# Kernel tuning notes

Measured on AMD Instinct MI355X. Metric: run time of the kernel, lower is better.

The kernel has to match this reference:

```python
import jax, jax.numpy as jnp
import numpy as np

B, S, D_IN, D_OUT = 4, 2048, 2048, 2048
E, R = 8, 8
SCALING = 16.0 / 8.0  # lora_alpha / r
# Dropout (p=0.05) treated as identity (eval mode) for a deterministic reference.

def setup_inputs() -> dict:
    key = jax.random.key(0)
    ks = jax.random.split(key, 8)
    x = jax.random.normal(ks[0], (B, S, D_IN), dtype=jnp.float32)
    base_W = jax.random.normal(ks[1], (D_OUT, D_IN), dtype=jnp.float32) * 0.02
    base_b = jax.random.normal(ks[2], (D_OUT,), dtype=jnp.float32) * 0.02
    shared_A = jax.random.normal(ks[3], (R, D_IN), dtype=jnp.float32) * 0.01
    shared_B = jax.random.normal(ks[4], (D_OUT, R), dtype=jnp.float32) * 0.01
    expert_A = jax.random.normal(ks[5], (E, R, D_IN), dtype=jnp.float32) * 0.01
    expert_B = jax.random.normal(ks[6], (E, D_OUT, R), dtype=jnp.float32) * 0.01
    task_emb = jax.random.normal(ks[7], (E, D_IN), dtype=jnp.float32) * 0.01
    collab_w = jnp.array(0.5, dtype=jnp.float32)
    return {"x": x, "base_W": base_W, "base_b": base_b,
            "shared_A": shared_A, "shared_B": shared_B,
            "expert_A": expert_A, "expert_B": expert_B,
            "task_emb": task_emb, "collab_w": collab_w}

def reference(x, base_W, base_b, shared_A, shared_B, expert_A, expert_B, task_emb, collab_w):
    # base linear: [B,S,D_out]
    base_out = jnp.einsum('bsi,oi->bso', x, base_W) + base_b
    # shared LoRA path
    shared_out = jnp.einsum('bsr,or->bso', jnp.einsum('bsi,ri->bsr', x, shared_A), shared_B) * SCALING
    # soft routing over task experts (task_id=None branch)
    x_mean = x.mean(axis=1)                               # [B,D_in]
    routing = jax.nn.softmax(x_mean @ task_emb.T, axis=-1)  # [B,E]
    t = jnp.einsum('bsi,eri->bser', x, expert_A)          # [B,S,E,R] low-rank
    task_out = jnp.einsum('bser,eor,be->bso', t, expert_B, routing) * SCALING
    cw = jax.nn.sigmoid(collab_w)
    return base_out + cw * shared_out + (1.0 - cw) * task_out
```

## Files before the change

kernel.cpp:

```cpp
#include <hip/hip_runtime.h>
#include <hip/hip_bf16.h>
#include <math.h>

#define BATCH 4
#define SEQ   2048
#define DIN   2048
#define DOUT  2048
#define NEXP  8
#define RANK  8
#define MTOT  (BATCH * SEQ)
#define KE    64

typedef __bf16 bf16x8 __attribute__((ext_vector_type(8)));
typedef __bf16 bf16x4 __attribute__((ext_vector_type(4)));
typedef float  f32x4  __attribute__((ext_vector_type(4)));

#define GLOBAL_AS __attribute__((address_space(1)))
#define LDS_AS    __attribute__((address_space(3)))

__global__ __launch_bounds__(256) void prep_all(
    const float* __restrict__ x, const float* __restrict__ W,
    const float* __restrict__ expert_A, const float* __restrict__ shared_A,
    const float* __restrict__ expert_B, const float* __restrict__ shared_B,
    const float* __restrict__ collab,
    __bf16* __restrict__ xb, float* __restrict__ partial,
    __bf16* __restrict__ Wb, __bf16* __restrict__ caug, __bf16* __restrict__ Ab)
{
    const int bid = blockIdx.x;
    const int t = threadIdx.x;
    if (bid < 1024) {
        const int dc = bid & 3, sc = (bid >> 2) & 63, b = bid >> 8;
        const int i = dc * 512 + t * 2;
        size_t base = ((size_t)b * SEQ + (size_t)sc * 32) * DIN + i;
        float a0 = 0.f, a1 = 0.f;
        for (int s = 0; s < 32; ++s) {
            float2 v = *(const float2*)&x[base + (size_t)s * DIN];
            a0 += v.x; a1 += v.y;
            __bf16 h0 = (__bf16)v.x, h1 = (__bf16)v.y;
            ((__bf16*)&xb[base + (size_t)s * DIN])[0] = h0;
            ((__bf16*)&xb[base + (size_t)s * DIN])[1] = h1;
        }
        float2 p = { a0, a1 };
        *(float2*)&partial[((size_t)b * 64 + sc) * DIN + i] = p;
    } else if (bid < 5120) {
        int idx = (bid - 1024) * 1024 + t * 4;
        int o = idx >> 11, i = idx & 2047;
        float cw = 1.0f / (1.0f + expf(-collab[0]));
        float s = cw * 2.0f;
        float4 w = *(const float4*)&W[idx];
        float dx = 0.f, dy = 0.f, dz = 0.f, dw = 0.f;
        #pragma unroll
        for (int r = 0; r < 8; ++r) {
            float bs = shared_B[(size_t)o * RANK + r];
            float4 as = *(const float4*)&shared_A[(size_t)r * DIN + i];
            dx += bs * as.x; dy += bs * as.y; dz += bs * as.z; dw += bs * as.w;
        }
        bf16x4 h = { (__bf16)(w.x + s * dx), (__bf16)(w.y + s * dy),
                     (__bf16)(w.z + s * dz), (__bf16)(w.w + s * dw) };
        *(bf16x4*)&Wb[idx] = h;
    } else if (bid < 5632) {
        int idx = (bid - 5120) * 256 + t;
        int k = idx & 63, o = idx >> 6;
        float cw = 1.0f / (1.0f + expf(-collab[0]));
        caug[idx] = (__bf16)((1.0f - cw) * 2.0f *
            expert_B[((size_t)(k >> 3) * DOUT + o) * RANK + (k & 7)]);
    } else {
        int idx = (bid - 5632) * 1024 + t * 4;
        float4 v = *(const float4*)&expert_A[idx];
        bf16x4 h = { (__bf16)v.x, (__bf16)v.y, (__bf16)v.z, (__bf16)v.w };
        *(bf16x4*)&Ab[idx] = h;
    }
}

__global__ __launch_bounds__(256) void gemm_t_rout(
    const __bf16* __restrict__ xb, const __bf16* __restrict__ Ab,
    const float* __restrict__ partial, const float* __restrict__ task_emb,
    __bf16* __restrict__ pt, float* __restrict__ routing)
{
    __shared__ __bf16 lsA[128 * 32];
    __shared__ __bf16 lsB[64 * 32];
    __shared__ float red[256];
    const int bid = blockIdx.x;
    const int t = threadIdx.x;

    if (bid >= 256) {
        const int b = bid - 256;
        float xm[8] = {0.f,0.f,0.f,0.f,0.f,0.f,0.f,0.f};
        for (int sc = 0; sc < 64; ++sc) {
            const float* pp = partial + ((size_t)b * 64 + sc) * DIN + t * 8;
            float4 v0 = *(const float4*)pp, v1 = *(const float4*)(pp + 4);
            xm[0] += v0.x; xm[1] += v0.y; xm[2] += v0.z; xm[3] += v0.w;
            xm[4] += v1.x; xm[5] += v1.y; xm[6] += v1.z; xm[7] += v1.w;
        }
        float le[NEXP];
        #pragma unroll
        for (int e = 0; e < NEXP; ++e) {
            const float* te = task_emb + (size_t)e * DIN + t * 8;
            float4 u0 = *(const float4*)te, u1 = *(const float4*)(te + 4);
            le[e] = xm[0]*u0.x + xm[1]*u0.y + xm[2]*u0.z + xm[3]*u0.w
                  + xm[4]*u1.x + xm[5]*u1.y + xm[6]*u1.z + xm[7]*u1.w;
        }
        __shared__ float logits[NEXP];
        for (int e = 0; e < NEXP; ++e) {
            red[t] = le[e];
            __syncthreads();
            for (int s = 128; s > 0; s >>= 1) {
                if (t < s) red[t] += red[t + s];
                __syncthreads();
            }
            if (t == 0) logits[e] = red[0] * (1.0f / (float)SEQ);
            __syncthreads();
        }
        if (t == 0) {
            float mx = logits[0];
            for (int e = 1; e < NEXP; ++e) mx = fmaxf(mx, logits[e]);
            float ex[NEXP], den = 0.f;
            for (int e = 0; e < NEXP; ++e) { ex[e] = expf(logits[e] - mx); den += ex[e]; }
            for (int e = 0; e < NEXP; ++e) routing[b * NEXP + e] = ex[e] / den;
        }
        return;
    }

    const int lane = t & 63;
    const int w = t >> 6;
    const int kc = bid & 3;
    const int m0 = (bid >> 2) * 128;

    f32x4 acc[2][4];
    #pragma unroll
    for (int a = 0; a < 2; ++a)
        #pragma unroll
        for (int c = 0; c < 4; ++c) acc[a][c] = (f32x4){0.f, 0.f, 0.f, 0.f};

    for (int k0 = kc * 512; k0 < kc * 512 + 512; k0 += 32) {
        #pragma unroll
        for (int q = 0; q < 2; ++q) {
            int L = q * 256 + t;
            int row = L >> 2, seg = L & 3;
            const __bf16* gpA = xb + (size_t)(m0 + row) * DIN + k0 + seg * 8;
            int Lu = q * 256 + (t & ~63);
            __builtin_amdgcn_global_load_lds((GLOBAL_AS void*)gpA,
                (LDS_AS void*)&lsA[Lu * 8], 16, 0, 0);
        }
        {
            int row = t >> 2, seg = t & 3;
            const __bf16* gpB = Ab + (size_t)row * DIN + k0 + seg * 8;
            __builtin_amdgcn_global_load_lds((GLOBAL_AS void*)gpB,
                (LDS_AS void*)&lsB[(t & ~63) * 8], 16, 0, 0);
        }
        __syncthreads();
        bf16x8 af[2], bfr[4];
        #pragma unroll
        for (int tm = 0; tm < 2; ++tm)
            af[tm] = *(const bf16x8*)&lsA[(w * 32 + tm * 16 + (lane & 15)) * 32 + (lane >> 4) * 8];
        #pragma unroll
        for (int tn = 0; tn < 4; ++tn)
            bfr[tn] = *(const bf16x8*)&lsB[(tn * 16 + (lane & 15)) * 32 + (lane >> 4) * 8];
        #pragma unroll
        for (int tm = 0; tm < 2; ++tm)
            #pragma unroll
            for (int tn = 0; tn < 4; ++tn)
                acc[tm][tn] = __builtin_amdgcn_mfma_f32_16x16x32_bf16(
                    af[tm], bfr[tn], acc[tm][tn], 0, 0, 0);
        __syncthreads();
    }
    #pragma unroll
    for (int tm = 0; tm < 2; ++tm)
        #pragma unroll
        for (int tn = 0; tn < 4; ++tn) {
            int col = tn * 16 + (lane & 15);
            #pragma unroll
            for (int v = 0; v < 4; ++v) {
                int row = m0 + w * 32 + tm * 16 + (lane >> 4) * 4 + v;
                pt[((size_t)kc * MTOT + row) * KE + col] = (__bf16)acc[tm][tn][v];
            }
        }
}

__global__ __launch_bounds__(256) void reduce_route(
    const __bf16* __restrict__ pt, const float* __restrict__ routing,
    __bf16* __restrict__ tb)
{
    size_t idx = ((size_t)blockIdx.x * 256 + threadIdx.x) * 4;
    int k0 = (int)(idx & 63);
    int m  = (int)(idx >> 6);
    int b  = m >> 11;
    float f = routing[b * NEXP + (k0 >> 3)];
    float sx = 0.f, sy = 0.f, sz = 0.f, sw = 0.f;
    #pragma unroll
    for (int kc = 0; kc < 4; ++kc) {
        bf16x4 v = *(const bf16x4*)&pt[(size_t)kc * MTOT * KE + idx];
        sx += (float)v[0]; sy += (float)v[1]; sz += (float)v[2]; sw += (float)v[3];
    }
    bf16x4 h = { (__bf16)(sx * f), (__bf16)(sy * f), (__bf16)(sz * f), (__bf16)(sw * f) };
    *(bf16x4*)&tb[idx] = h;
}

__global__ __launch_bounds__(256) void gemm_main(
    const __bf16* __restrict__ xb, const __bf16* __restrict__ Wb,
    const __bf16* __restrict__ tb, const __bf16* __restrict__ caug,
    const float* __restrict__ bias, float* __restrict__ out)
{
    __shared__ __bf16 lsA[128 * 64];
    __shared__ __bf16 lsB[128 * 64];
    const int t = threadIdx.x;
    const int lane = t & 63;
    const int wm = (t >> 6) >> 1, wn = (t >> 6) & 1;
    const int m0 = blockIdx.x * 128;
    const int n0 = blockIdx.y * 128;

    int rowq[4], segq[4], ldso[4];
    #pragma unroll
    for (int q = 0; q < 4; ++q) {
        rowq[q] = q * 32 + (t >> 3);
        segq[q] = (t & 7) ^ (rowq[q] & 7);
        ldso[q] = (q * 256 + (t & ~63)) * 8;
    }
    const __bf16* pA[4]; const __bf16* pB[4];
    #pragma unroll
    for (int q = 0; q < 4; ++q) {
        pA[q] = xb + (size_t)(m0 + rowq[q]) * DIN + segq[q] * 8;
        pB[q] = Wb + (size_t)(n0 + rowq[q]) * DIN + segq[q] * 8;
    }
    int aoff[2][4], boff[2][4];
    #pragma unroll
    for (int tm = 0; tm < 4; ++tm) {
        int r = wm * 64 + tm * 16 + (lane & 15);
        #pragma unroll
        for (int kk = 0; kk < 2; ++kk)
            aoff[kk][tm] = r * 64 + (((kk * 4 + (lane >> 4)) ^ (r & 7)) * 8);
    }
    #pragma unroll
    for (int tn = 0; tn < 4; ++tn) {
        int r = wn * 64 + tn * 16 + (lane & 15);
        #pragma unroll
        for (int kk = 0; kk < 2; ++kk)
            boff[kk][tn] = r * 64 + (((kk * 4 + (lane >> 4)) ^ (r & 7)) * 8);
    }

    f32x4 acc[4][4];
    #pragma unroll
    for (int a = 0; a < 4; ++a)
        #pragma unroll
        for (int c = 0; c < 4; ++c) acc[a][c] = (f32x4){0.f, 0.f, 0.f, 0.f};

    for (int it = 0; it < 32; ++it) {
        #pragma unroll
        for (int q = 0; q < 4; ++q) {
            __builtin_amdgcn_global_load_lds((GLOBAL_AS void*)pA[q],
                (LDS_AS void*)&lsA[ldso[q]], 16, 0, 0);
            __builtin_amdgcn_global_load_lds((GLOBAL_AS void*)pB[q],
                (LDS_AS void*)&lsB[ldso[q]], 16, 0, 0);
            pA[q] += 64; pB[q] += 64;
        }
        __syncthreads();
        #pragma unroll
        for (int kk = 0; kk < 2; ++kk) {
            bf16x8 af[4], bfr[4];
            #pragma unroll
            for (int tm = 0; tm < 4; ++tm) af[tm]  = *(const bf16x8*)&lsA[aoff[kk][tm]];
            #pragma unroll
            for (int tn = 0; tn < 4; ++tn) bfr[tn] = *(const bf16x8*)&lsB[boff[kk][tn]];
            #pragma unroll
            for (int tm = 0; tm < 4; ++tm)
                #pragma unroll
                for (int tn = 0; tn < 4; ++tn)
                    acc[tm][tn] = __builtin_amdgcn_mfma_f32_16x16x32_bf16(
                        af[tm], bfr[tn], acc[tm][tn], 0, 0, 0);
        }
        __syncthreads();
    }

    {
        #pragma unroll
        for (int q = 0; q < 4; ++q) {
            const __bf16* qA = tb   + (size_t)(m0 + rowq[q]) * KE + segq[q] * 8;
            const __bf16* qB = caug + (size_t)(n0 + rowq[q]) * KE + segq[q] * 8;
            __builtin_amdgcn_global_load_lds((GLOBAL_AS void*)qA,
                (LDS_AS void*)&lsA[ldso[q]], 16, 0, 0);
            __builtin_amdgcn_global_load_lds((GLOBAL_AS void*)qB,
                (LDS_AS void*)&lsB[ldso[q]], 16, 0, 0);
        }
        __syncthreads();
        #pragma unroll
        for (int kk = 0; kk < 2; ++kk) {
            bf16x8 af[4], bfr[4];
            #pragma unroll
            for (int tm = 0; tm < 4; ++tm) af[tm]  = *(const bf16x8*)&lsA[aoff[kk][tm]];
            #pragma unroll
            for (int tn = 0; tn < 4; ++tn) bfr[tn] = *(const bf16x8*)&lsB[boff[kk][tn]];
            #pragma unroll
            for (int tm = 0; tm < 4; ++tm)
                #pragma unroll
                for (int tn = 0; tn < 4; ++tn)
                    acc[tm][tn] = __builtin_amdgcn_mfma_f32_16x16x32_bf16(
                        af[tm], bfr[tn], acc[tm][tn], 0, 0, 0);
        }
        __syncthreads();
    }

    #pragma unroll
    for (int tm = 0; tm < 4; ++tm)
        #pragma unroll
        for (int tn = 0; tn < 4; ++tn) {
            int col = n0 + wn * 64 + tn * 16 + (lane & 15);
            float bv = bias[col];
            #pragma unroll
            for (int v = 0; v < 4; ++v) {
                int row = m0 + wm * 64 + tm * 16 + (lane >> 4) * 4 + v;
                out[(size_t)row * DOUT + col] = acc[tm][tn][v] + bv;
            }
        }
}

extern "C" void kernel_launch(void* const* d_in, const int* in_sizes, int n_in,
                              void* d_out, int out_size, void* d_ws, size_t ws_size,
                              hipStream_t stream)
{
    const float* x        = (const float*)d_in[0];
    const float* base_W   = (const float*)d_in[1];
    const float* base_b   = (const float*)d_in[2];
    const float* shared_A = (const float*)d_in[3];
    const float* shared_B = (const float*)d_in[4];
    const float* expert_A = (const float*)d_in[5];
    const float* expert_B = (const float*)d_in[6];
    const float* task_emb = (const float*)d_in[7];
    const float* collab_w = (const float*)d_in[8];
    float* out = (float*)d_out;

    char* ws = (char*)d_ws;
    __bf16* xb      = (__bf16*)(ws + 0);
    __bf16* Wb      = (__bf16*)(ws + 33554432);
    __bf16* pt      = (__bf16*)(ws + 41943040);
    __bf16* tb      = (__bf16*)(ws + 46137344);
    __bf16* caug    = (__bf16*)(ws + 47185920);
    __bf16* Ab      = (__bf16*)(ws + 47448064);
    float*  partial = (float*) (ws + 47710208);
    float*  routing = (float*) (ws + 49807360);

    prep_all    <<<dim3(5760), 256, 0, stream>>>(x, base_W, expert_A, shared_A,
                                                 expert_B, shared_B, collab_w,
                                                 xb, partial, Wb, caug, Ab);
    gemm_t_rout <<<dim3(260), 256, 0, stream>>>(xb, Ab, partial, task_emb, pt, routing);
    reduce_route<<<dim3(512), 256, 0, stream>>>(pt, routing, tb);
    gemm_main   <<<dim3(64, 16), 256, 0, stream>>>(xb, Wb, tb, caug, base_b, out);
}
```

Before: 242.4 us.

## Fold routing logits into low-rank GEMM and fuse reduce into main GEMM

Drops the separate x-mean pass and routing block. task_emb is appended as extra rows of the low-rank A matrix, so routing logits fall out of the t-GEMM by linearity and are accumulated with atomics. The reduce_route kernel is removed: gemm_main sums the four split-K partials, computes the softmax and scales the A fragments in registers before the expert MFMA step. The low-rank GEMM also moves to a 64-wide K tile with swizzled LDS, and the x conversion is vectorised. One launch and several intermediate buffers go away, at the cost of an extra memset, atomics, and bf16 precision for the mean/logit path.

```diff
diff --git a/kernel.cpp b/kernel.cpp
--- a/kernel.cpp
+++ b/kernel.cpp
@@ -10,6 +10,7 @@
 #define RANK  8
 #define MTOT  (BATCH * SEQ)
 #define KE    64
+#define KAB   96
 
 typedef __bf16 bf16x8 __attribute__((ext_vector_type(8)));
 typedef __bf16 bf16x4 __attribute__((ext_vector_type(4)));
@@ -22,29 +23,25 @@
     const float* __restrict__ x, const float* __restrict__ W,
     const float* __restrict__ expert_A, const float* __restrict__ shared_A,
     const float* __restrict__ expert_B, const float* __restrict__ shared_B,
-    const float* __restrict__ collab,
-    __bf16* __restrict__ xb, float* __restrict__ partial,
-    __bf16* __restrict__ Wb, __bf16* __restrict__ caug, __bf16* __restrict__ Ab)
+    const float* __restrict__ task_emb, const float* __restrict__ collab,
+    __bf16* __restrict__ xb, __bf16* __restrict__ Wb,
+    __bf16* __restrict__ caug, __bf16* __restrict__ Ab)
 {
     const int bid = blockIdx.x;
     const int t = threadIdx.x;
-    if (bid < 1024) {
-        const int dc = bid & 3, sc = (bid >> 2) & 63, b = bid >> 8;
-        const int i = dc * 512 + t * 2;
-        size_t base = ((size_t)b * SEQ + (size_t)sc * 32) * DIN + i;
-        float a0 = 0.f, a1 = 0.f;
-        for (int s = 0; s < 32; ++s) {
-            float2 v = *(const float2*)&x[base + (size_t)s * DIN];
-            a0 += v.x; a1 += v.y;
-            __bf16 h0 = (__bf16)v.x, h1 = (__bf16)v.y;
-            ((__bf16*)&xb[base + (size_t)s * DIN])[0] = h0;
-            ((__bf16*)&xb[base + (size_t)s * DIN])[1] = h1;
-        }
-        float2 p = { a0, a1 };
-        *(float2*)&partial[((size_t)b * 64 + sc) * DIN + i] = p;
-    } else if (bid < 5120) {
-        int idx = (bid - 1024) * 1024 + t * 4;
-        int o = idx >> 11, i = idx & 2047;
+    if (bid < 2048) {
+        size_t base = (size_t)bid * 8192 + (size_t)t * 32;
+        #pragma unroll
+        for (int j = 0; j < 4; ++j) {
+            float4 v0 = *(const float4*)&x[base + j * 8];
+            float4 v1 = *(const float4*)&x[base + j * 8 + 4];
+            bf16x8 h = { (__bf16)v0.x, (__bf16)v0.y, (__bf16)v0.z, (__bf16)v0.w,
+                         (__bf16)v1.x, (__bf16)v1.y, (__bf16)v1.z, (__bf16)v1.w };
+            *(bf16x8*)&xb[base + j * 8] = h;
+        }
+    } else if (bid < 6144) {
+        size_t idx = (size_t)(bid - 2048) * 1024 + t * 4;
+        int o = (int)(idx >> 11), i = (int)(idx & 2047);
         float cw = 1.0f / (1.0f + expf(-collab[0]));
         float s = cw * 2.0f;
         float4 w = *(const float4*)&W[idx];
@@ -58,112 +55,99 @@
         bf16x4 h = { (__bf16)(w.x + s * dx), (__bf16)(w.y + s * dy),
                      (__bf16)(w.z + s * dz), (__bf16)(w.w + s * dw) };
         *(bf16x4*)&Wb[idx] = h;
-    } else if (bid < 5632) {
-        int idx = (bid - 5120) * 256 + t;
-        int k = idx & 63, o = idx >> 6;
+    } else if (bid < 6272) {
+        int idx = (bid - 6144) * 1024 + t * 4;
+        int o = idx >> 6, k = idx & 63;
         float cw = 1.0f / (1.0f + expf(-collab[0]));
-        caug[idx] = (__bf16)((1.0f - cw) * 2.0f *
-            expert_B[((size_t)(k >> 3) * DOUT + o) * RANK + (k & 7)]);
+        float s = (1.0f - cw) * 2.0f;
+        float4 v = *(const float4*)&expert_B[((size_t)(k >> 3) * DOUT + o) * RANK + (k & 7)];
+        bf16x4 h = { (__bf16)(s * v.x), (__bf16)(s * v.y),
+                     (__bf16)(s * v.z), (__bf16)(s * v.w) };
+        *(bf16x4*)&caug[idx] = h;
     } else {
-        int idx = (bid - 5632) * 1024 + t * 4;
-        float4 v = *(const float4*)&expert_A[idx];
-        bf16x4 h = { (__bf16)v.x, (__bf16)v.y, (__bf16)v.z, (__bf16)v.w };
-        *(bf16x4*)&Ab[idx] = h;
+        int row = bid - 6272;
+        int c = t * 8;
+        bf16x8 h = { (__bf16)0.f, (__bf16)0.f, (__bf16)0.f, (__bf16)0.f,
+                     (__bf16)0.f, (__bf16)0.f, (__bf16)0.f, (__bf16)0.f };
+        if (row < 64) {
+            float4 v0 = *(const float4*)&expert_A[(size_t)row * DIN + c];
+            float4 v1 = *(const float4*)&expert_A[(size_t)row * DIN + c + 4];
+            h = bf16x8{ (__bf16)v0.x, (__bf16)v0.y, (__bf16)v0.z, (__bf16)v0.w,
+                        (__bf16)v1.x, (__bf16)v1.y, (__bf16)v1.z, (__bf16)v1.w };
+        } else if (row < 72) {
+            float4 v0 = *(const float4*)&task_emb[(size_t)(row - 64) * DIN + c];
+            float4 v1 = *(const float4*)&task_emb[(size_t)(row - 64) * DIN + c + 4];
+            h = bf16x8{ (__bf16)v0.x, (__bf16)v0.y, (__bf16)v0.z, (__bf16)v0.w,
+                        (__bf16)v1.x, (__bf16)v1.y, (__bf16)v1.z, (__bf16)v1.w };
+        }
+        *(bf16x8*)&Ab[(size_t)row * DIN + c] = h;
     }
 }
 
-__global__ __launch_bounds__(256) void gemm_t_rout(
+__global__ __launch_bounds__(256) void gemm_t(
     const __bf16* __restrict__ xb, const __bf16* __restrict__ Ab,
-    const float* __restrict__ partial, const float* __restrict__ task_emb,
-    __bf16* __restrict__ pt, float* __restrict__ routing)
+    __bf16* __restrict__ pt, float* __restrict__ logits)
 {
-    __shared__ __bf16 lsA[128 * 32];
-    __shared__ __bf16 lsB[64 * 32];
-    __shared__ float red[256];
+    __shared__ __bf16 lsA[128 * 64];
+    __shared__ __bf16 lsB[KAB * 64];
+    __shared__ float lsc[32];
     const int bid = blockIdx.x;
     const int t = threadIdx.x;
-
-    if (bid >= 256) {
-        const int b = bid - 256;
-        float xm[8] = {0.f,0.f,0.f,0.f,0.f,0.f,0.f,0.f};
-        for (int sc = 0; sc < 64; ++sc) {
-            const float* pp = partial + ((size_t)b * 64 + sc) * DIN + t * 8;
-            float4 v0 = *(const float4*)pp, v1 = *(const float4*)(pp + 4);
-            xm[0] += v0.x; xm[1] += v0.y; xm[2] += v0.z; xm[3] += v0.w;
-            xm[4] += v1.x; xm[5] += v1.y; xm[6] += v1.z; xm[7] += v1.w;
-        }
-        float le[NEXP];
-        #pragma unroll
-        for (int e = 0; e < NEXP; ++e) {
-            const float* te = task_emb + (size_t)e * DIN + t * 8;
-            float4 u0 = *(const float4*)te, u1 = *(const float4*)(te + 4);
-            le[e] = xm[0]*u0.x + xm[1]*u0.y + xm[2]*u0.z + xm[3]*u0.w
-                  + xm[4]*u1.x + xm[5]*u1.y + xm[6]*u1.z + xm[7]*u1.w;
-        }
-        __shared__ float logits[NEXP];
-        for (int e = 0; e < NEXP; ++e) {
-            red[t] = le[e];
-            __syncthreads();
-            for (int s = 128; s > 0; s >>= 1) {
-                if (t < s) red[t] += red[t + s];
-                __syncthreads();
-            }
-            if (t == 0) logits[e] = red[0] * (1.0f / (float)SEQ);
-            __syncthreads();
-        }
-        if (t == 0) {
-            float mx = logits[0];
-            for (int e = 1; e < NEXP; ++e) mx = fmaxf(mx, logits[e]);
-            float ex[NEXP], den = 0.f;
-            for (int e = 0; e < NEXP; ++e) { ex[e] = expf(logits[e] - mx); den += ex[e]; }
-            for (int e = 0; e < NEXP; ++e) routing[b * NEXP + e] = ex[e] / den;
-        }
-        return;
-    }
-
     const int lane = t & 63;
     const int w = t >> 6;
     const int kc = bid & 3;
     const int m0 = (bid >> 2) * 128;
-
-    f32x4 acc[2][4];
+    const int b  = bid >> 6;
+
+    f32x4 acc[2][5];
     #pragma unroll
     for (int a = 0; a < 2; ++a)
         #pragma unroll
-        for (int c = 0; c < 4; ++c) acc[a][c] = (f32x4){0.f, 0.f, 0.f, 0.f};
-
-    for (int k0 = kc * 512; k0 < kc * 512 + 512; k0 += 32) {
-        #pragma unroll
-        for (int q = 0; q < 2; ++q) {
-            int L = q * 256 + t;
-            int row = L >> 2, seg = L & 3;
-            const __bf16* gpA = xb + (size_t)(m0 + row) * DIN + k0 + seg * 8;
-            int Lu = q * 256 + (t & ~63);
-            __builtin_amdgcn_global_load_lds((GLOBAL_AS void*)gpA,
-                (LDS_AS void*)&lsA[Lu * 8], 16, 0, 0);
-        }
-        {
-            int row = t >> 2, seg = t & 3;
-            const __bf16* gpB = Ab + (size_t)row * DIN + k0 + seg * 8;
-            __builtin_amdgcn_global_load_lds((GLOBAL_AS void*)gpB,
-                (LDS_AS void*)&lsB[(t & ~63) * 8], 16, 0, 0);
-        }
-        __syncthreads();
-        bf16x8 af[2], bfr[4];
-        #pragma unroll
-        for (int tm = 0; tm < 2; ++tm)
-            af[tm] = *(const bf16x8*)&lsA[(w * 32 + tm * 16 + (lane & 15)) * 32 + (lane >> 4) * 8];
-        #pragma unroll
-        for (int tn = 0; tn < 4; ++tn)
-            bfr[tn] = *(const bf16x8*)&lsB[(tn * 16 + (lane & 15)) * 32 + (lane >> 4) * 8];
-        #pragma unroll
-        for (int tm = 0; tm < 2; ++tm)
-            #pragma unroll
-            for (int tn = 0; tn < 4; ++tn)
-                acc[tm][tn] = __builtin_amdgcn_mfma_f32_16x16x32_bf16(
-                    af[tm], bfr[tn], acc[tm][tn], 0, 0, 0);
-        __syncthreads();
-    }
+        for (int c = 0; c < 5; ++c) acc[a][c] = (f32x4){0.f, 0.f, 0.f, 0.f};
+
+    for (int k0 = kc * 512; k0 < kc * 512 + 512; k0 += 64) {
+        #pragma unroll
+        for (int q = 0; q < 4; ++q) {
+            int G = q * 256 + t;
+            int row = G >> 3, sl = G & 7, seg = sl ^ (row & 7);
+            const __bf16* gp = xb + (size_t)(m0 + row) * DIN + k0 + seg * 8;
+            __builtin_amdgcn_global_load_lds((GLOBAL_AS void*)gp,
+                (LDS_AS void*)&lsA[(q * 256 + (t & ~63)) * 8], 16, 0, 0);
+        }
+        #pragma unroll
+        for (int q = 0; q < 3; ++q) {
+            int G = q * 256 + t;
+            int row = G >> 3, sl = G & 7, seg = sl ^ (row & 7);
+            const __bf16* gp = Ab + (size_t)row * DIN + k0 + seg * 8;
+            __builtin_amdgcn_global_load_lds((GLOBAL_AS void*)gp,
+                (LDS_AS void*)&lsB[(q * 256 + (t & ~63)) * 8], 16, 0, 0);
+        }
+        __syncthreads();
+        #pragma unroll
+        for (int kk = 0; kk < 2; ++kk) {
+            bf16x8 af[2], bfr[5];
+            #pragma unroll
+            for (int tm = 0; tm < 2; ++tm) {
+                int r = w * 32 + tm * 16 + (lane & 15);
+                int slot = (kk * 4 + (lane >> 4)) ^ (r & 7);
+                af[tm] = *(const bf16x8*)&lsA[r * 64 + slot * 8];
+            }
+            #pragma unroll
+            for (int tn = 0; tn < 5; ++tn) {
+                int r = tn * 16 + (lane & 15);
+                int slot = (kk * 4 + (lane >> 4)) ^ (r & 7);
+                bfr[tn] = *(const bf16x8*)&lsB[r * 64 + slot * 8];
+            }
+            #pragma unroll
+            for (int tm = 0; tm < 2; ++tm)
+                #pragma unroll
+                for (int tn = 0; tn < 5; ++tn)
+                    acc[tm][tn] = __builtin_amdgcn_mfma_f32_16x16x32_bf16(
+                        af[tm], bfr[tn], acc[tm][tn], 0, 0, 0);
+        }
+        __syncthreads();
+    }
+
     #pragma unroll
     for (int tm = 0; tm < 2; ++tm)
         #pragma unroll
@@ -175,31 +159,27 @@
                 pt[((size_t)kc * MTOT + row) * KE + col] = (__bf16)acc[tm][tn][v];
             }
         }
-}
-
-__global__ __launch_bounds__(256) void reduce_route(
-    const __bf16* __restrict__ pt, const float* __restrict__ routing,
-    __bf16* __restrict__ tb)
-{
-    size_t idx = ((size_t)blockIdx.x * 256 + threadIdx.x) * 4;
-    int k0 = (int)(idx & 63);
-    int m  = (int)(idx >> 6);
-    int b  = m >> 11;
-    float f = routing[b * NEXP + (k0 >> 3)];
-    float sx = 0.f, sy = 0.f, sz = 0.f, sw = 0.f;
-    #pragma unroll
-    for (int kc = 0; kc < 4; ++kc) {
-        bf16x4 v = *(const bf16x4*)&pt[(size_t)kc * MTOT * KE + idx];
-        sx += (float)v[0]; sy += (float)v[1]; sz += (float)v[2]; sw += (float)v[3];
-    }
-    bf16x4 h = { (__bf16)(sx * f), (__bf16)(sy * f), (__bf16)(sz * f), (__bf16)(sw * f) };
-    *(bf16x4*)&tb[idx] = h;
+
+    float s = 0.f;
+    #pragma unroll
+    for (int tm = 0; tm < 2; ++tm)
+        #pragma unroll
+        for (int v = 0; v < 4; ++v) s += acc[tm][4][v];
+    s += __shfl_down(s, 32);
+    s += __shfl_down(s, 16);
+    if (lane < 8) lsc[w * 8 + lane] = s;
+    __syncthreads();
+    if (t < 8) {
+        float tot = lsc[t] + lsc[8 + t] + lsc[16 + t] + lsc[24 + t];
+        atomicAdd(&logits[b * NEXP + t], tot);
+    }
 }
 
 __global__ __launch_bounds__(256) void gemm_main(
     const __bf16* __restrict__ xb, const __bf16* __restrict__ Wb,
-    const __bf16* __restrict__ tb, const __bf16* __restrict__ caug,
-    const float* __restrict__ bias, float* __restrict__ out)
+    const __bf16* __restrict__ pt, const __bf16* __restrict__ caug,
+    const float* __restrict__ logits, const float* __restrict__ bias,
+    float* __restrict__ out)
 {
     __shared__ __bf16 lsA[128 * 64];
     __shared__ __bf16 lsB[128 * 64];
@@ -208,6 +188,23 @@
     const int wm = (t >> 6) >> 1, wn = (t >> 6) & 1;
     const int m0 = blockIdx.x * 128;
     const int n0 = blockIdx.y * 128;
+    const int b  = m0 >> 11;
+
+    float f[NEXP];
+    {
+        float li[NEXP];
+        #pragma unroll
+        for (int e = 0; e < NEXP; ++e) li[e] = logits[b * NEXP + e] * (1.0f / (float)SEQ);
+        float mx = li[0];
+        #pragma unroll
+        for (int e = 1; e < NEXP; ++e) mx = fmaxf(mx, li[e]);
+        float den = 0.f;
+        #pragma unroll
+        for (int e = 0; e < NEXP; ++e) { f[e] = expf(li[e] - mx); den += f[e]; }
+        float rden = 1.0f / den;
+        #pragma unroll
+        for (int e = 0; e < NEXP; ++e) f[e] *= rden;
+    }
 
     int rowq[4], segq[4], ldso[4];
     #pragma unroll
@@ -216,34 +213,74 @@
         segq[q] = (t & 7) ^ (rowq[q] & 7);
         ldso[q] = (q * 256 + (t & ~63)) * 8;
     }
+    int aoff[2][4], boff[2][4];
+    #pragma unroll
+    for (int tm = 0; tm < 4; ++tm) {
+        int r = wm * 64 + tm * 16 + (lane & 15);
+        #pragma unroll
+        for (int kk = 0; kk < 2; ++kk)
+            aoff[kk][tm] = r * 64 + (((kk * 4 + (lane >> 4)) ^ (r & 7)) * 8);
+    }
+    #pragma unroll
+    for (int tn = 0; tn < 4; ++tn) {
+        int r = wn * 64 + tn * 16 + (lane & 15);
+        #pragma unroll
+        for (int kk = 0; kk < 2; ++kk)
+            boff[kk][tn] = r * 64 + (((kk * 4 + (lane >> 4)) ^ (r & 7)) * 8);
+    }
+
+    f32x4 acc[4][4];
+    #pragma unroll
+    for (int a = 0; a < 4; ++a)
+        #pragma unroll
+        for (int c = 0; c < 4; ++c) acc[a][c] = (f32x4){0.f, 0.f, 0.f, 0.f};
+
+    {
+        #pragma unroll
+        for (int q = 0; q < 4; ++q) {
+            const __bf16* gp = caug + (size_t)(n0 + rowq[q]) * KE + segq[q] * 8;
+            __builtin_amdgcn_global_load_lds((GLOBAL_AS void*)gp,
+                (LDS_AS void*)&lsB[ldso[q]], 16, 0, 0);
+        }
+        __syncthreads();
+        #pragma unroll
+        for (int kk = 0; kk < 2; ++kk) {
+            float fe = f[kk * 4 + (lane >> 4)];
+            bf16x8 afc[4], bfr[4];
+            #pragma unroll
+            for (int tm = 0; tm < 4; ++tm) {
+                int rm = m0 + wm * 64 + tm * 16 + (lane & 15);
+                int kb = kk * 32 + (lane >> 4) * 8;
+                const __bf16* p0 = pt + (size_t)rm * KE + kb;
+                bf16x8 v0 = *(const bf16x8*)(p0);
+                bf16x8 v1 = *(const bf16x8*)(p0 + (size_t)MTOT * KE);
+                bf16x8 v2 = *(const bf16x8*)(p0 + (size_t)2 * MTOT * KE);
+                bf16x8 v3 = *(const bf16x8*)(p0 + (size_t)3 * MTOT * KE);
+                bf16x8 r;
+                #pragma unroll
+                for (int j = 0; j < 8; ++j)
+                    r[j] = (__bf16)(((float)v0[j] + (float)v1[j] +
+                                     (float)v2[j] + (float)v3[j]) * fe);
+                afc[tm] = r;
+            }
+            #pragma unroll
+            for (int tn = 0; tn < 4; ++tn) bfr[tn] = *(const bf16x8*)&lsB[boff[kk][tn]];
+            #pragma unroll
+            for (int tm = 0; tm < 4; ++tm)
+                #pragma unroll
+                for (int tn = 0; tn < 4; ++tn)
+                    acc[tm][tn] = __builtin_amdgcn_mfma_f32_16x16x32_bf16(
+                        afc[tm], bfr[tn], acc[tm][tn], 0, 0, 0);
+        }
+        __syncthreads();
+    }
+
     const __bf16* pA[4]; const __bf16* pB[4];
     #pragma unroll
     for (int q = 0; q < 4; ++q) {
         pA[q] = xb + (size_t)(m0 + rowq[q]) * DIN + segq[q] * 8;
         pB[q] = Wb + (size_t)(n0 + rowq[q]) * DIN + segq[q] * 8;
     }
-    int aoff[2][4], boff[2][4];
-    #pragma unroll
-    for (int tm = 0; tm < 4; ++tm) {
-        int r = wm * 64 + tm * 16 + (lane & 15);
-        #pragma unroll
-        for (int kk = 0; kk < 2; ++kk)
-            aoff[kk][tm] = r * 64 + (((kk * 4 + (lane >> 4)) ^ (r & 7)) * 8);
-    }
-    #pragma unroll
-    for (int tn = 0; tn < 4; ++tn) {
-        int r = wn * 64 + tn * 16 + (lane & 15);
-        #pragma unroll
-        for (int kk = 0; kk < 2; ++kk)
-            boff[kk][tn] = r * 64 + (((kk * 4 + (lane >> 4)) ^ (r & 7)) * 8);
-    }
-
-    f32x4 acc[4][4];
-    #pragma unroll
-    for (int a = 0; a < 4; ++a)
-        #pragma unroll
-        for (int c = 0; c < 4; ++c) acc[a][c] = (f32x4){0.f, 0.f, 0.f, 0.f};
-
     for (int it = 0; it < 32; ++it) {
         #pragma unroll
         for (int q = 0; q < 4; ++q) {
@@ -252,34 +289,6 @@
             __builtin_amdgcn_global_load_lds((GLOBAL_AS void*)pB[q],
                 (LDS_AS void*)&lsB[ldso[q]], 16, 0, 0);
             pA[q] += 64; pB[q] += 64;
-        }
-        __syncthreads();
-        #pragma unroll
-        for (int kk = 0; kk < 2; ++kk) {
-            bf16x8 af[4], bfr[4];
-            #pragma unroll
-            for (int tm = 0; tm < 4; ++tm) af[tm]  = *(const bf16x8*)&lsA[aoff[kk][tm]];
-            #pragma unroll
-            for (int tn = 0; tn < 4; ++tn) bfr[tn] = *(const bf16x8*)&lsB[boff[kk][tn]];
-            #pragma unroll
-            for (int tm = 0; tm < 4; ++tm)
-                #pragma unroll
-                for (int tn = 0; tn < 4; ++tn)
-                    acc[tm][tn] = __builtin_amdgcn_mfma_f32_16x16x32_bf16(
-                        af[tm], bfr[tn], acc[tm][tn], 0, 0, 0);
-        }
-        __syncthreads();
-    }
-
-    {
-        #pragma unroll
-        for (int q = 0; q < 4; ++q) {
-            const __bf16* qA = tb   + (size_t)(m0 + rowq[q]) * KE + segq[q] * 8;
-            const __bf16* qB = caug + (size_t)(n0 + rowq[q]) * KE + segq[q] * 8;
-            __builtin_amdgcn_global_load_lds((GLOBAL_AS void*)qA,
-                (LDS_AS void*)&lsA[ldso[q]], 16, 0, 0);
-            __builtin_amdgcn_global_load_lds((GLOBAL_AS void*)qB,
-                (LDS_AS void*)&lsB[ldso[q]], 16, 0, 0);
         }
         __syncthreads();
         #pragma unroll
@@ -329,19 +338,17 @@
     float* out = (float*)d_out;
 
     char* ws = (char*)d_ws;
-    __bf16* xb      = (__bf16*)(ws + 0);
-    __bf16* Wb      = (__bf16*)(ws + 33554432);
-    __bf16* pt      = (__bf16*)(ws + 41943040);
-    __bf16* tb      = (__bf16*)(ws + 46137344);
-    __bf16* caug    = (__bf16*)(ws + 47185920);
-    __bf16* Ab      = (__bf16*)(ws + 47448064);
-    float*  partial = (float*) (ws + 47710208);
-    float*  routing = (float*) (ws + 49807360);
-
-    prep_all    <<<dim3(5760), 256, 0, stream>>>(x, base_W, expert_A, shared_A,
-                                                 expert_B, shared_B, collab_w,
-                                                 xb, partial, Wb, caug, Ab);
-    gemm_t_rout <<<dim3(260), 256, 0, stream>>>(xb, Ab, partial, task_emb, pt, routing);
-    reduce_route<<<dim3(512), 256, 0, stream>>>(pt, routing, tb);
-    gemm_main   <<<dim3(64, 16), 256, 0, stream>>>(xb, Wb, tb, caug, base_b, out);
+    __bf16* xb     = (__bf16*)(ws + 0);
+    __bf16* Wb     = (__bf16*)(ws + 33554432);
+    __bf16* pt     = (__bf16*)(ws + 41943040);
+    __bf16* caug   = (__bf16*)(ws + 46137344);
+    __bf16* Ab     = (__bf16*)(ws + 46399488);
+    float*  logits = (float*) (ws + 46792704);
+
+    hipMemsetAsync(logits, 0, 256, stream);
+    prep_all <<<dim3(6368), 256, 0, stream>>>(x, base_W, expert_A, shared_A,
+                                              expert_B, shared_B, task_emb, collab_w,
+                                              xb, Wb, caug, Ab);
+    gemm_t   <<<dim3(256), 256, 0, stream>>>(xb, Ab, pt, logits);
+    gemm_main<<<dim3(64, 16), 256, 0, stream>>>(xb, Wb, pt, caug, logits, base_b, out);
 }
```

Result: slower. 257.2 us (+6.1%).
